# Performance work log

Hardware: AMD Instinct MI355X
Metric: run time of the kernel (lower is better)

The kernel has to match this reference:

```python
import jax, jax.numpy as jnp
import numpy as np

# sym2 (== db2) decomposition filters from pywt
_DEC_LO = np.array([-0.12940952255126037, 0.22414386804185735,
                    0.8365163037378079, 0.48296291314453416], dtype=np.float32)
_DEC_HI = np.array([-0.48296291314453416, 0.8365163037378079,
                    -0.22414386804185735, -0.12940952255126037], dtype=np.float32)
# pytorch_wavelets flips the filters before torch's cross-correlation conv
H0R = jnp.asarray(_DEC_LO[::-1].copy())
H1R = jnp.asarray(_DEC_HI[::-1].copy())
L = 4  # filter length
LEVEL = 3


def afb1d(x):
    """One level of DWT (mode='zero'), x: (B, C, N) -> (lo, hi) each (B, C, (N+L-1)//2)."""
    N = x.shape[-1]
    out = (N + L - 1) // 2              # pywt dwt_coeff_len for mode='zero'
    p = 2 * (out - 1) - N + L           # total pad
    if p % 2 == 1:                      # odd-length signals get one extra zero at the end
        x = jnp.pad(x, ((0, 0), (0, 0), (0, 1)))
    ph = p // 2
    x = jnp.pad(x, ((0, 0), (0, 0), (ph, ph)))
    # strided windows: y[n] = sum_k h[k] * x_pad[2n + k]
    wins = [x[..., k:k + 2 * out:2][..., :out] for k in range(L)]
    lo = sum(H0R[k] * wins[k] for k in range(L))
    hi = sum(H1R[k] * wins[k] for k in range(L))
    return lo, hi


def wavelet_packet(x, level=LEVEL):
    # breadth-first, lo-first ordering == lexicographic sort of 'a'/'d' paths
    bands = [x]
    for _ in range(level):
        nxt = []
        for b in bands:
            lo, hi = afb1d(b)
            nxt.append(lo)
            nxt.append(hi)
        bands = nxt
    return bands


def setup_inputs() -> dict:
    key = jax.random.key(0)
    k1, k2, k3 = jax.random.split(key, 3)
    B, C, N, num_classes = 131072, 3, 50, 5
    total_features = 192  # 8 leaves * 3 channels * 8 samples
    x = jax.random.normal(k1, (B, C, N), dtype=jnp.float32)
    W = jax.random.normal(k2, (num_classes, total_features), dtype=jnp.float32) * 0.05
    b = jax.random.normal(k3, (num_classes,), dtype=jnp.float32) * 0.05
    return {"x": x, "W": W, "b": b}


def reference(x, W, b):
    bands = wavelet_packet(x)
    B = x.shape[0]
    feats = jnp.concatenate([band.reshape(B, -1) for band in bands], axis=1)  # (B, 192)
    return feats @ W.T + b                          # (B, 5)
```

## Files before the change

kernel.cpp:

```cpp
#include <hip/hip_runtime.h>

struct Amat { float a[64][50]; };

constexpr Amat makeA() {
    constexpr float h0[4] = { 0.48296291314453416f,  0.8365163037378079f,
                              0.22414386804185735f, -0.12940952255126037f};
    constexpr float h1[4] = {-0.12940952255126037f, -0.22414386804185735f,
                              0.8365163037378079f,  -0.48296291314453416f};
    float L1[2][26][50] = {};
    for (int band = 0; band < 2; ++band)
        for (int m = 0; m < 26; ++m)
            for (int n = 0; n < 50; ++n) {
                int k = n - 2 * m + 2;
                L1[band][m][n] = (k >= 0 && k < 4) ? (band ? h1[k] : h0[k]) : 0.0f;
            }
    float L2[4][14][50] = {};
    for (int j = 0; j < 4; ++j)
        for (int m = 0; m < 14; ++m)
            for (int n = 0; n < 50; ++n) {
                float acc = 0.0f;
                for (int k = 0; k < 4; ++k) {
                    int p = 2 * m + k - 2;
                    if (p >= 0 && p < 26)
                        acc += (j & 1 ? h1[k] : h0[k]) * L1[j >> 1][p][n];
                }
                L2[j][m][n] = acc;
            }
    Amat A = {};
    for (int j = 0; j < 8; ++j)
        for (int m = 0; m < 8; ++m)
            for (int n = 0; n < 50; ++n) {
                float acc = 0.0f;
                for (int k = 0; k < 4; ++k) {
                    int p = 2 * m + k - 2;
                    if (p >= 0 && p < 14)
                        acc += (j & 1 ? h1[k] : h0[k]) * L2[j >> 1][p][n];
                }
                A.a[j * 8 + m][n] = acc;
            }
    return A;
}

__device__ __constant__ Amat cA = makeA();

#define SWP 193

#define FMA_EL(xv, ib)                          \
    a0 = fmaf(sM[(ib) * 5 + 0], (xv), a0);      \
    a1 = fmaf(sM[(ib) * 5 + 1], (xv), a1);      \
    a2 = fmaf(sM[(ib) * 5 + 2], (xv), a2);      \
    a3 = fmaf(sM[(ib) * 5 + 3], (xv), a3);      \
    a4 = fmaf(sM[(ib) * 5 + 4], (xv), a4);

__global__ __launch_bounds__(256) void dwt_fused(const float* __restrict__ x,
                                                 const float* __restrict__ W,
                                                 const float* __restrict__ bias,
                                                 float* __restrict__ out) {
    __shared__ float sW[5 * SWP];
    __shared__ float sM[752];
    const int tid = threadIdx.x;
    const size_t g   = (size_t)blockIdx.x * 256 + tid;
    const size_t row = g >> 2;
    const int    q   = (int)(g & 3);

    const float2* __restrict__ xr = (const float2*)(x + row * 150);

    float2 v[19];
    #pragma unroll
    for (int j = 0; j < 18; ++j) v[j] = xr[4 * j + q];
    v[18] = xr[(q < 3) ? (72 + q) : 74];

    #pragma unroll
    for (int t = 0; t < 4; ++t) {
        const int idx = tid + t * 256;
        if (idx < 960) sW[(idx / 192) * SWP + (idx % 192)] = W[idx];
    }
    __syncthreads();

    #pragma unroll
    for (int t = 0; t < 3; ++t) {
        const int p = tid + t * 256;
        if (p < 750) {
            const int i = p / 5, k = p - 5 * i;
            const int c = i / 50, n = i - 50 * c;
            float acc = 0.f;
            #pragma unroll 16
            for (int f = 0; f < 64; ++f)
                acc = fmaf(sW[k * SWP + (f >> 3) * 24 + c * 8 + (f & 7)],
                           cA.a[f][n], acc);
            sM[p] = acc;
        }
    }
    __syncthreads();

    float a0 = 0.f, a1 = 0.f, a2 = 0.f, a3 = 0.f, a4 = 0.f;
    #pragma unroll
    for (int j = 0; j < 18; ++j) {
        const int ib = 2 * (4 * j + q);
        FMA_EL(v[j].x, ib)
        FMA_EL(v[j].y, ib + 1)
    }
    if (q < 3) {
        const int ib = 2 * (72 + q);
        FMA_EL(v[18].x, ib)
        FMA_EL(v[18].y, ib + 1)
    }

    a0 += __shfl_xor(a0, 1); a0 += __shfl_xor(a0, 2);
    a1 += __shfl_xor(a1, 1); a1 += __shfl_xor(a1, 2);
    a2 += __shfl_xor(a2, 1); a2 += __shfl_xor(a2, 2);
    a3 += __shfl_xor(a3, 1); a3 += __shfl_xor(a3, 2);
    a4 += __shfl_xor(a4, 1); a4 += __shfl_xor(a4, 2);

    if (q == 0) {
        float* o = out + row * 5;
        o[0] = a0 + bias[0];
        o[1] = a1 + bias[1];
        o[2] = a2 + bias[2];
        o[3] = a3 + bias[3];
        o[4] = a4 + bias[4];
    }
}

extern "C" void kernel_launch(void* const* d_in, const int* in_sizes, int n_in,
                              void* d_out, int out_size, void* d_ws, size_t ws_size,
                              hipStream_t stream) {
    const float* x    = (const float*)d_in[0];
    const float* W    = (const float*)d_in[1];
    const float* bias = (const float*)d_in[2];
    float*       out  = (float*)d_out;

    const int B = in_sizes[0] / 150;
    const int grid = (B * 4) / 256;
    dwt_fused<<<grid, 256, 0, stream>>>(x, W, bias, out);
}
```

Measured before the change: 30.55 us.

## Precompute fused wavelet-linear matrix once in a setup kernel, then run streaming GEMV

```diff
diff --git a/kernel.cpp b/kernel.cpp
--- a/kernel.cpp
+++ b/kernel.cpp
@@ -43,68 +43,84 @@
 
 __device__ __constant__ Amat cA = makeA();
 
-#define SWP 193
+__global__ __launch_bounds__(256) void build_M(const float* __restrict__ W,
+                                               const float* __restrict__ bias,
+                                               float* __restrict__ Mgt) {
+    __shared__ float sW[960];
+    const int tid = threadIdx.x;
+    #pragma unroll
+    for (int t = 0; t < 4; ++t) {
+        const int idx = tid + t * 256;
+        if (idx < 960) sW[idx] = W[idx];
+    }
+    __syncthreads();
 
-#define FMA_EL(xv, ib)                          \
-    a0 = fmaf(sM[(ib) * 5 + 0], (xv), a0);      \
-    a1 = fmaf(sM[(ib) * 5 + 1], (xv), a1);      \
-    a2 = fmaf(sM[(ib) * 5 + 2], (xv), a2);      \
-    a3 = fmaf(sM[(ib) * 5 + 3], (xv), a3);      \
-    a4 = fmaf(sM[(ib) * 5 + 4], (xv), a4);
+    if (tid < 150) {
+        const int c = tid / 50, n = tid - c * 50;
+        float m0 = 0.f, m1 = 0.f, m2 = 0.f, m3 = 0.f, m4 = 0.f;
+        #pragma unroll 16
+        for (int f = 0; f < 64; ++f) {
+            const float av = cA.a[f][n];
+            const int wj = (f >> 3) * 24 + c * 8 + (f & 7);
+            m0 = fmaf(sW[0 * 192 + wj], av, m0);
+            m1 = fmaf(sW[1 * 192 + wj], av, m1);
+            m2 = fmaf(sW[2 * 192 + wj], av, m2);
+            m3 = fmaf(sW[3 * 192 + wj], av, m3);
+            m4 = fmaf(sW[4 * 192 + wj], av, m4);
+        }
+        Mgt[0 * 152 + tid] = m0;
+        Mgt[1 * 152 + tid] = m1;
+        Mgt[2 * 152 + tid] = m2;
+        Mgt[3 * 152 + tid] = m3;
+        Mgt[4 * 152 + tid] = m4;
+    } else if (tid < 155) {
+        const int k = tid - 150;
+        Mgt[k * 152 + 150] = bias[k];
+    } else if (tid < 160) {
+        const int k = tid - 155;
+        Mgt[k * 152 + 151] = 0.f;
+    }
+}
 
-__global__ __launch_bounds__(256) void dwt_fused(const float* __restrict__ x,
-                                                 const float* __restrict__ W,
-                                                 const float* __restrict__ bias,
-                                                 float* __restrict__ out) {
-    __shared__ float sW[5 * SWP];
-    __shared__ float sM[752];
+#define QSTEP(fi)                                                        \
+    {   const float2 xv = xr[(fi)];                                      \
+        const int ib = 2 * (fi);                                         \
+        { const float2 mm = *(const float2*)&sMt[0 * 152 + ib];          \
+          a0 = fmaf(mm.x, xv.x, a0); a0 = fmaf(mm.y, xv.y, a0); }        \
+        { const float2 mm = *(const float2*)&sMt[1 * 152 + ib];          \
+          a1 = fmaf(mm.x, xv.x, a1); a1 = fmaf(mm.y, xv.y, a1); }        \
+        { const float2 mm = *(const float2*)&sMt[2 * 152 + ib];          \
+          a2 = fmaf(mm.x, xv.x, a2); a2 = fmaf(mm.y, xv.y, a2); }        \
+        { const float2 mm = *(const float2*)&sMt[3 * 152 + ib];          \
+          a3 = fmaf(mm.x, xv.x, a3); a3 = fmaf(mm.y, xv.y, a3); }        \
+        { const float2 mm = *(const float2*)&sMt[4 * 152 + ib];          \
+          a4 = fmaf(mm.x, xv.x, a4); a4 = fmaf(mm.y, xv.y, a4); }        \
+    }
+
+__global__ __launch_bounds__(256, 4) void dwt_gemv(const float* __restrict__ x,
+                                                   const float* __restrict__ Mgt,
+                                                   float* __restrict__ out) {
+    __shared__ float sMt[5 * 152];
     const int tid = threadIdx.x;
+    #pragma unroll
+    for (int t = 0; t < 3; ++t) {
+        const int idx = tid + t * 256;
+        if (idx < 760) sMt[idx] = Mgt[idx];
+    }
+    __syncthreads();
+
     const size_t g   = (size_t)blockIdx.x * 256 + tid;
     const size_t row = g >> 2;
     const int    q   = (int)(g & 3);
-
     const float2* __restrict__ xr = (const float2*)(x + row * 150);
 
-    float2 v[19];
-    #pragma unroll
-    for (int j = 0; j < 18; ++j) v[j] = xr[4 * j + q];
-    v[18] = xr[(q < 3) ? (72 + q) : 74];
+    float a0 = 0.f, a1 = 0.f, a2 = 0.f, a3 = 0.f, a4 = 0.f;
 
     #pragma unroll
-    for (int t = 0; t < 4; ++t) {
-        const int idx = tid + t * 256;
-        if (idx < 960) sW[(idx / 192) * SWP + (idx % 192)] = W[idx];
-    }
-    __syncthreads();
-
-    #pragma unroll
-    for (int t = 0; t < 3; ++t) {
-        const int p = tid + t * 256;
-        if (p < 750) {
-            const int i = p / 5, k = p - 5 * i;
-            const int c = i / 50, n = i - 50 * c;
-            float acc = 0.f;
-            #pragma unroll 16
-            for (int f = 0; f < 64; ++f)
-                acc = fmaf(sW[k * SWP + (f >> 3) * 24 + c * 8 + (f & 7)],
-                           cA.a[f][n], acc);
-            sM[p] = acc;
-        }
-    }
-    __syncthreads();
-
-    float a0 = 0.f, a1 = 0.f, a2 = 0.f, a3 = 0.f, a4 = 0.f;
-    #pragma unroll
-    for (int j = 0; j < 18; ++j) {
-        const int ib = 2 * (4 * j + q);
-        FMA_EL(v[j].x, ib)
-        FMA_EL(v[j].y, ib + 1)
-    }
-    if (q < 3) {
-        const int ib = 2 * (72 + q);
-        FMA_EL(v[18].x, ib)
-        FMA_EL(v[18].y, ib + 1)
-    }
+    for (int j = 0; j < 18; ++j)
+        QSTEP(4 * j + q)
+    if (q < 3)
+        QSTEP(72 + q)
 
     a0 += __shfl_xor(a0, 1); a0 += __shfl_xor(a0, 2);
     a1 += __shfl_xor(a1, 1); a1 += __shfl_xor(a1, 2);
@@ -114,11 +130,11 @@
 
     if (q == 0) {
         float* o = out + row * 5;
-        o[0] = a0 + bias[0];
-        o[1] = a1 + bias[1];
-        o[2] = a2 + bias[2];
-        o[3] = a3 + bias[3];
-        o[4] = a4 + bias[4];
+        o[0] = a0 + sMt[0 * 152 + 150];
+        o[1] = a1 + sMt[1 * 152 + 150];
+        o[2] = a2 + sMt[2 * 152 + 150];
+        o[3] = a3 + sMt[3 * 152 + 150];
+        o[4] = a4 + sMt[4 * 152 + 150];
     }
 }
 
@@ -129,8 +145,11 @@
     const float* W    = (const float*)d_in[1];
     const float* bias = (const float*)d_in[2];
     float*       out  = (float*)d_out;
+    float*       Mgt  = (float*)d_ws;
+
+    build_M<<<1, 256, 0, stream>>>(W, bias, Mgt);
 
     const int B = in_sizes[0] / 150;
     const int grid = (B * 4) / 256;
-    dwt_fused<<<grid, 256, 0, stream>>>(x, W, bias, out);
+    dwt_gemv<<<grid, 256, 0, stream>>>(x, Mgt, out);
 }
```

Result: faster. 25.16 us (-17.6%).
